# Kernel optimization log

Measured on AMD Instinct MI355X. Metric: run time of the kernel, lower is better.

Reference implementation:

```python
import jax, jax.numpy as jnp
import numpy as np
from jax import lax

V, T, B, E, H, L, K = 32000, 256, 32, 512, 256, 2, 17  # vocab, seq, batch, emb, hidden/dir, layers, tags


def _lstm_dir(x, mask, Wih, Whh, bih, bhh, reverse):
    """One-direction LSTM with packed-sequence semantics.
    x: [B,T,D], mask: [B,T] bool. Padded steps do not update (h,c); padded outputs are 0."""
    Bs, Ts, _ = x.shape
    Hs = Whh.shape[1]
    xg = jnp.einsum('btd,gd->btg', x, Wih) + bih  # precompute input contributions [B,T,4H]

    def step(carry, inp):
        h, c = carry
        xg_t, m_t = inp  # [B,4H], [B]
        g = xg_t + h @ Whh.T + bhh
        i, f, gg, o = jnp.split(g, 4, axis=-1)  # torch gate order: i, f, g, o
        i = jax.nn.sigmoid(i); f = jax.nn.sigmoid(f)
        gg = jnp.tanh(gg); o = jax.nn.sigmoid(o)
        c_new = f * c + i * gg
        h_new = o * jnp.tanh(c_new)
        m = m_t[:, None]
        h2 = jnp.where(m, h_new, h)
        c2 = jnp.where(m, c_new, c)
        out = jnp.where(m, h_new, jnp.zeros_like(h_new))
        return (h2, c2), out

    z = jnp.zeros((Bs, Hs), dtype=x.dtype)
    xs = (jnp.swapaxes(xg, 0, 1), mask.T)
    _, ys = lax.scan(step, (z, z), xs, reverse=reverse)
    return jnp.swapaxes(ys, 0, 1)  # [B,T,H]


def _bilstm(x, mask, Wih, Whh, bih, bhh):
    for l in range(Wih.shape[0]):
        f = _lstm_dir(x, mask, Wih[l, 0], Whh[l, 0], bih[l, 0], bhh[l, 0], reverse=False)
        b = _lstm_dir(x, mask, Wih[l, 1], Whh[l, 1], bih[l, 1], bhh[l, 1], reverse=True)
        x = jnp.concatenate([f, b], axis=-1)
    return x


def _crf_nll(logits, labels, mask, input_lens, trans, start, end):
    maskf = mask.astype(logits.dtype)
    # --- numerator: score of gold path (AllenNLP _joint_likelihood) ---
    emit = jnp.take_along_axis(logits, labels[..., None], axis=2)[..., 0]  # [B,T]
    emit_sum = (emit * maskf).sum(1)
    tr = trans[labels[:, :-1], labels[:, 1:]]  # [B,T-1]
    tr_sum = (tr * maskf[:, 1:]).sum(1)
    last_tags = jnp.take_along_axis(labels, (input_lens - 1)[:, None], axis=1)[:, 0]
    numerator = start[labels[:, 0]] + emit_sum + tr_sum + end[last_tags]
    # --- denominator: forward algorithm over time ---
    alpha0 = start[None, :] + logits[:, 0]  # [B,K]

    def step(alpha, inp):
        logit_t, m_t = inp  # [B,K], [B]
        inner = alpha[:, :, None] + trans[None] + logit_t[:, None, :]  # [B,K,K]
        new = jax.nn.logsumexp(inner, axis=1)
        alpha = jnp.where(m_t[:, None], new, alpha)
        return alpha, None

    xs = (jnp.swapaxes(logits[:, 1:], 0, 1), mask[:, 1:].T)
    alpha, _ = lax.scan(step, alpha0, xs)
    partition = jax.nn.logsumexp(alpha + end[None, :], axis=1)
    return -(numerator - partition).sum()


def setup_inputs() -> dict:
    key = jax.random.key(0)
    ks = jax.random.split(key, 10)
    lens = jax.random.randint(ks[0], (B,), 1, T + 1)
    src = jax.random.randint(ks[1], (B, T), 1, V)
    src = jnp.where(jnp.arange(T)[None, :] < lens[:, None], src, 0)  # pad_idx=0
    labels = jax.random.randint(ks[2], (B, T), 0, K)
    emb = (jax.random.normal(ks[3], (V, E)) * 0.05).at[0].set(0.0)  # padding_idx=0 row zeroed
    Wih = jax.random.normal(ks[4], (L, 2, 4 * H, E)) * 0.05
    Whh = jax.random.normal(ks[5], (L, 2, 4 * H, H)) * 0.05
    bih = jnp.zeros((L, 2, 4 * H))
    bhh = jnp.zeros((L, 2, 4 * H))
    Wlin = jax.random.normal(ks[6], (K, 2 * H)) * 0.05
    blin = jnp.zeros((K,))
    trans = jax.random.normal(ks[7], (K, K)) * 0.05
    start = jax.random.normal(ks[8], (K,)) * 0.05
    end = jax.random.normal(ks[9], (K,)) * 0.05
    return dict(src=src, input_lens=lens, labels=labels, decode=0, emb=emb,
                Wih=Wih, Whh=Whh, bih=bih, bhh=bhh, Wlin=Wlin, blin=blin,
                trans=trans, start=start, end=end)


def reference(src, input_lens, labels, decode, emb, Wih, Whh, bih, bhh, Wlin, blin, trans, start, end):
    mask = src != 0  # create_mask with pad_idx=0
    x = emb[src]  # embedding lookup (dropout p=0 -> identity)
    feats = _bilstm(x, mask, Wih, Whh, bih, bhh)
    logits = feats @ Wlin.T + blin  # [B,T,K]
    # decode=False path: loss = -crf log-likelihood (summed over batch)
    return _crf_nll(logits, labels, mask, input_lens, trans, start, end)
```

## Files before the change

### kernel.cpp

```cpp
#include <hip/hip_runtime.h>

#define TT 256
#define BB 32
#define EE 512
#define HH 256
#define GG 1024
#define NK 17

typedef __attribute__((ext_vector_type(8))) short bf16x8;
typedef __attribute__((ext_vector_type(4))) float f32x4;

#if __has_builtin(__builtin_amdgcn_sdot8)
#define HAS_DOT8 1
#else
#define HAS_DOT8 0
#endif

__device__ __forceinline__ int dot4i8(int a, int b, int c) {
#if __has_builtin(__builtin_amdgcn_sdot4)
  return __builtin_amdgcn_sdot4(a, b, c, false);
#else
  int r = c;
#pragma unroll
  for (int e = 0; e < 4; ++e) {
    int av = (a << (24 - 8 * e)) >> 24;
    int bv = (b << (24 - 8 * e)) >> 24;
    r += av * bv;
  }
  return r;
#endif
}

__device__ __forceinline__ int dot8i4(int a, int b, int c) {
#if HAS_DOT8
  return __builtin_amdgcn_sdot8(a, b, c, false);
#else
  int alo = (a << 4) & (int)0xF0F0F0F0, ahi = a & (int)0xF0F0F0F0;
  int blo = (b << 4) & (int)0xF0F0F0F0, bhi = b & (int)0xF0F0F0F0;
  c = dot4i8(alo, blo, c);
  return dot4i8(ahi, bhi, c);
#endif
}

__device__ __forceinline__ short f2bf(float f) {
  unsigned int u = __float_as_uint(f);
  unsigned int rounding = 0x7FFFu + ((u >> 16) & 1u);
  return (short)((u + rounding) >> 16);
}
__device__ __forceinline__ float bfu2f_lo(unsigned int u) {
  return __uint_as_float(u << 16);
}
__device__ __forceinline__ float bfu2f_hi(unsigned int u) {
  return __uint_as_float(u & 0xFFFF0000u);
}
__device__ __forceinline__ float bfs2f(unsigned short us) {
  return __uint_as_float(((unsigned int)us) << 16);
}

__global__ void k_prep_x(const int* __restrict__ src,
                         const float* __restrict__ emb,
                         const float* __restrict__ Wih,
                         short* __restrict__ xb,
                         short* __restrict__ wbb) {
  int blk = blockIdx.x;
  int t = threadIdx.x;
  if (blk < BB * TT) {
    int v = src[blk];
    const float4* e = reinterpret_cast<const float4*>(emb + (size_t)v * EE) + 2 * t;
    float4 a = e[0], b = e[1];
    bf16x8 r;
    r[0] = f2bf(a.x); r[1] = f2bf(a.y); r[2] = f2bf(a.z); r[3] = f2bf(a.w);
    r[4] = f2bf(b.x); r[5] = f2bf(b.y); r[6] = f2bf(b.z); r[7] = f2bf(b.w);
    *reinterpret_cast<bf16x8*>(xb + (size_t)blk * EE + 8 * t) = r;
  } else {
    int i = ((blk - BB * TT) * 64 + t) * 8;
    float4 a = *reinterpret_cast<const float4*>(Wih + i);
    float4 b = *reinterpret_cast<const float4*>(Wih + i + 4);
    bf16x8 r;
    r[0] = f2bf(a.x); r[1] = f2bf(a.y); r[2] = f2bf(a.z); r[3] = f2bf(a.w);
    r[4] = f2bf(b.x); r[5] = f2bf(b.y); r[6] = f2bf(b.z); r[7] = f2bf(b.w);
    *reinterpret_cast<bf16x8*>(wbb + i) = r;
  }
}

__global__ __launch_bounds__(256) void k_quant4(const float* __restrict__ whh,
                                                const float* __restrict__ bih,
                                                const float* __restrict__ bhh,
                                                int* __restrict__ wq4,
                                                float* __restrict__ scl,
                                                float* __restrict__ biasb) {
  int wid = (blockIdx.x * 256 + threadIdx.x) >> 6;
  int lane = threadIdx.x & 63;
  int ld = wid >> 10, g = wid & 1023;
  float4 v = *reinterpret_cast<const float4*>(whh + (size_t)wid * HH + lane * 4);
  float m = fmaxf(fmaxf(fabsf(v.x), fabsf(v.y)), fmaxf(fabsf(v.z), fabsf(v.w)));
#pragma unroll
  for (int off = 32; off > 0; off >>= 1) m = fmaxf(m, __shfl_xor(m, off));
  m = fmaxf(m, 1e-20f);
  float inv = 7.f / m;
  unsigned q0 = (unsigned)((int)rintf(v.x * inv) & 0xF);
  unsigned q1 = (unsigned)((int)rintf(v.y * inv) & 0xF);
  unsigned q2 = (unsigned)((int)rintf(v.z * inv) & 0xF);
  unsigned q3 = (unsigned)((int)rintf(v.w * inv) & 0xF);
  unsigned bits = q0 | (q1 << 4) | (q2 << 8) | (q3 << 12);
  unsigned hi = __shfl_down(bits, 1);
  if (!(lane & 1)) {
    int kk = lane >> 1;
    wq4[(((size_t)ld * 8 + (kk >> 2)) * 1024 + g) * 4 + (kk & 3)] =
        (int)(bits | (hi << 16));
  }
  if (lane == 0) scl[wid] = m / 49.f;
  if (lane == 1) biasb[wid] = bih[wid] + bhh[wid];
}

__global__ __launch_bounds__(256) void k_gemm_mfma(
    const short* __restrict__ Xb,
    const short* __restrict__ Wb,
    const float* __restrict__ bias,
    unsigned short* __restrict__ out) {
  __shared__ short As[128][72];
  __shared__ short Bs[128][72];
  const int tid = threadIdx.x;
  const int wave = tid >> 6, lane = tid & 63;
  const int wr = wave >> 1, wc = wave & 1;
  const int m0 = blockIdx.y * 128, n0 = blockIdx.x * 128;
  f32x4 acc[4][4] = {};
  for (int k0 = 0; k0 < EE; k0 += 64) {
#pragma unroll
    for (int u = 0; u < 4; ++u) {
      int cid = u * 256 + tid;
      int row = cid >> 3, kc = cid & 7;
      *reinterpret_cast<int4*>(&As[row][kc * 8]) =
          *reinterpret_cast<const int4*>(Xb + (size_t)(m0 + row) * EE + k0 + kc * 8);
      *reinterpret_cast<int4*>(&Bs[row][kc * 8]) =
          *reinterpret_cast<const int4*>(Wb + (size_t)(n0 + row) * EE + k0 + kc * 8);
    }
    __syncthreads();
#pragma unroll
    for (int ko = 0; ko < 2; ++ko) {
      bf16x8 af[4], bff[4];
#pragma unroll
      for (int mi = 0; mi < 4; ++mi)
        af[mi] = *reinterpret_cast<const bf16x8*>(
            &As[wr * 64 + mi * 16 + (lane & 15)][ko * 32 + (lane >> 4) * 8]);
#pragma unroll
      for (int ni = 0; ni < 4; ++ni)
        bff[ni] = *reinterpret_cast<const bf16x8*>(
            &Bs[wc * 64 + ni * 16 + (lane & 15)][ko * 32 + (lane >> 4) * 8]);
#pragma unroll
      for (int mi = 0; mi < 4; ++mi)
#pragma unroll
        for (int ni = 0; ni < 4; ++ni)
          acc[mi][ni] = __builtin_amdgcn_mfma_f32_16x16x32_bf16(af[mi], bff[ni], acc[mi][ni], 0, 0, 0);
    }
    __syncthreads();
  }
  const int r0 = (lane >> 4) * 4, cc = lane & 15;
#pragma unroll
  for (int mi = 0; mi < 4; ++mi)
#pragma unroll
    for (int ni = 0; ni < 4; ++ni) {
      int gcol = n0 + wc * 64 + ni * 16 + cc;
      int dir = gcol >> 10, gg = gcol & 1023;
      float bv = bias[gcol];
      unsigned short* ob = out + (size_t)dir * (BB * TT * GG) + gg;
#pragma unroll
      for (int j = 0; j < 4; ++j) {
        int m = m0 + wr * 64 + mi * 16 + r0 + j;
        ob[(size_t)m * GG] = (unsigned short)f2bf(acc[mi][ni][j] + bv);
      }
    }
}

__global__ __launch_bounds__(512, 2) void k_rec(
    const unsigned short* __restrict__ xg,
    const uint4* __restrict__ wq4,
    const float* __restrict__ scl,
    const int* __restrict__ lens,
    short* __restrict__ outx)
{
  __shared__ float pre[GG];
  __shared__ __align__(16) int hq[32];
  const int bid = blockIdx.x;
  const int b = bid & 31;
  const int dir = bid >> 5;
  const int L = threadIdx.x;
  const int g0 = L, g1 = L + 512;
  const uint4* wp0 = wq4 + (size_t)dir * (8 * 1024) + g0;
  const uint4* wp1 = wq4 + (size_t)dir * (8 * 1024) + g1;
  if (L < 32) hq[L] = 0;
#if HAS_DOT8
  const float f0 = scl[dir * 1024 + g0];
  const float f1 = scl[dir * 1024 + g1];
#else
  const float f0 = scl[dir * 1024 + g0] * (1.f / 256.f);
  const float f1 = scl[dir * 1024 + g1] * (1.f / 256.f);
#endif
  const int len = lens[b];
  const unsigned short* xgb = xg + ((size_t)dir * (BB * TT) + (size_t)b * TT) * GG;
  float c = 0.f;
  __syncthreads();
  for (int s = 0; s < TT; ++s) {
    const int t = dir ? (TT - 1 - s) : s;
    float xv0 = bfs2f(xgb[(size_t)t * GG + g0]);
    float xv1 = bfs2f(xgb[(size_t)t * GG + g1]);
    const uint4* h4 = reinterpret_cast<const uint4*>(hq);
    uint4 hv0 = h4[0], hv1 = h4[1], hv2 = h4[2], hv3 = h4[3];
    uint4 hv4 = h4[4], hv5 = h4[5], hv6 = h4[6], hv7 = h4[7];
    int a0 = 0, a1 = 0;
#define DOTQ(WP, ACC, Q, HV)                               \
    { uint4 wv = WP[(Q) * 1024];                           \
      ACC = dot8i4((int)wv.x, (int)HV.x, ACC);             \
      ACC = dot8i4((int)wv.y, (int)HV.y, ACC);             \
      ACC = dot8i4((int)wv.z, (int)HV.z, ACC);             \
      ACC = dot8i4((int)wv.w, (int)HV.w, ACC); }
    DOTQ(wp0, a0, 0, hv0) DOTQ(wp0, a0, 1, hv1)
    DOTQ(wp0, a0, 2, hv2) DOTQ(wp0, a0, 3, hv3)
    DOTQ(wp0, a0, 4, hv4) DOTQ(wp0, a0, 5, hv5)
    DOTQ(wp0, a0, 6, hv6) DOTQ(wp0, a0, 7, hv7)
    DOTQ(wp1, a1, 0, hv0) DOTQ(wp1, a1, 1, hv1)
    DOTQ(wp1, a1, 2, hv2) DOTQ(wp1, a1, 3, hv3)
    DOTQ(wp1, a1, 4, hv4) DOTQ(wp1, a1, 5, hv5)
    DOTQ(wp1, a1, 6, hv6) DOTQ(wp1, a1, 7, hv7)
#undef DOTQ
    pre[g0] = xv0 + (float)a0 * f0;
    pre[g1] = xv1 + (float)a1 * f1;
    __syncthreads();
    if (L < HH) {
      float gi = pre[L], gf = pre[HH + L], g2 = pre[2 * HH + L], go = pre[3 * HH + L];
      float iv = 1.f / (1.f + __expf(-gi));
      float fv = 1.f / (1.f + __expf(-gf));
      float e2 = __expf(fminf(2.f * g2, 80.f));
      float gv = (e2 - 1.f) / (e2 + 1.f);
      float ov = 1.f / (1.f + __expf(-go));
      float cn = fv * c + iv * gv;
      float e2c = __expf(fminf(2.f * cn, 80.f));
      float th = (e2c - 1.f) / (e2c + 1.f);
      float hn = ov * th;
      const bool m = (t < len);
      outx[((size_t)(b * TT) + t) * (2 * HH) + dir * HH + L] = f2bf(m ? hn : 0.f);
      if (m) {
        c = cn;
        int nib = ((int)rintf(hn * 7.f)) & 0xF;
        int pn = __shfl_xor(nib, 1);
        if (!(L & 1))
          reinterpret_cast<char*>(hq)[L >> 1] = (char)(nib | (pn << 4));
      }
    }
    __syncthreads();
  }
}

__global__ __launch_bounds__(256) void k_logits(
    const short* __restrict__ feats,
    const float* __restrict__ wlin,
    const float* __restrict__ blin,
    float* __restrict__ logits) {
  int o = blockIdx.x * 256 + threadIdx.x;
  int m = o / NK, jj = o - m * NK;
  const uint4* fr = reinterpret_cast<const uint4*>(feats + (size_t)m * EE);
  const float4* wr = reinterpret_cast<const float4*>(wlin + (size_t)jj * EE);
  float s = blin[jj];
  for (int q = 0; q < EE / 8; ++q) {
    uint4 fv = fr[q];
    float4 w0 = wr[2 * q], w1 = wr[2 * q + 1];
    s = fmaf(bfu2f_lo(fv.x), w0.x, s);
    s = fmaf(bfu2f_hi(fv.x), w0.y, s);
    s = fmaf(bfu2f_lo(fv.y), w0.z, s);
    s = fmaf(bfu2f_hi(fv.y), w0.w, s);
    s = fmaf(bfu2f_lo(fv.z), w1.x, s);
    s = fmaf(bfu2f_hi(fv.z), w1.y, s);
    s = fmaf(bfu2f_lo(fv.w), w1.z, s);
    s = fmaf(bfu2f_hi(fv.w), w1.w, s);
  }
  logits[o] = s;
}

__global__ __launch_bounds__(64) void k_crf(
    const float* __restrict__ logits,
    const int* __restrict__ labels,
    const int* __restrict__ lens,
    const float* __restrict__ trans,
    const float* __restrict__ startv,
    const float* __restrict__ endv,
    float* __restrict__ res) {
  const int b = blockIdx.x;
  const int tid = threadIdx.x;
  __shared__ float trs[NK * NK];
  __shared__ float alpha[NK];
  for (int i = tid; i < NK * NK; i += 64) trs[i] = trans[i];
  const int len = lens[b];
  const int* lab = labels + b * TT;
  const float* lg = logits + (size_t)b * TT * NK;
  float part = 0.f;
  for (int t = tid; t < TT; t += 64)
    if (t < len) part += lg[t * NK + lab[t]];
  for (int t = tid; t < TT - 1; t += 64)
    if (t + 1 < len) part += trs[lab[t] * NK + lab[t + 1]];
#pragma unroll
  for (int off = 32; off > 0; off >>= 1) part += __shfl_down(part, off);
  if (tid < NK) alpha[tid] = startv[tid] + lg[tid];
  const int tmax = (len < TT) ? len : TT;
  for (int t = 1; t < tmax; ++t) {
    float nv = 0.f;
    if (tid < NK) {
      float mxv = -1e30f;
#pragma unroll
      for (int i = 0; i < NK; ++i) mxv = fmaxf(mxv, alpha[i] + trs[i * NK + tid]);
      float sum = 0.f;
#pragma unroll
      for (int i = 0; i < NK; ++i) sum += __expf(alpha[i] + trs[i * NK + tid] - mxv);
      nv = mxv + __logf(sum) + lg[t * NK + tid];
    }
    if (tid < NK) alpha[tid] = nv;
  }
  if (tid == 0) {
    float mxv = -1e30f;
    float av[NK];
    for (int i = 0; i < NK; ++i) { av[i] = alpha[i] + endv[i]; mxv = fmaxf(mxv, av[i]); }
    float sum = 0.f;
    for (int i = 0; i < NK; ++i) sum += __expf(av[i] - mxv);
    float partition = mxv + __logf(sum);
    float numer = startv[lab[0]] + part + endv[lab[len - 1]];
    res[b] = numer - partition;
  }
}

__global__ void k_final(const float* __restrict__ res, float* __restrict__ out) {
  int tid = threadIdx.x;
  float v = (tid < BB) ? res[tid] : 0.f;
#pragma unroll
  for (int off = 32; off > 0; off >>= 1) v += __shfl_down(v, off);
  if (tid == 0) out[0] = -v;
}

extern "C" void kernel_launch(void* const* d_in, const int* in_sizes, int n_in,
                              void* d_out, int out_size, void* d_ws, size_t ws_size,
                              hipStream_t stream) {
  const int* src = (const int*)d_in[0];
  const int* lens = (const int*)d_in[1];
  const int* labels = (const int*)d_in[2];
  const float* emb = (const float*)d_in[4];
  const float* Wih = (const float*)d_in[5];
  const float* Whh = (const float*)d_in[6];
  const float* bih = (const float*)d_in[7];
  const float* bhh = (const float*)d_in[8];
  const float* Wlin = (const float*)d_in[9];
  const float* blin = (const float*)d_in[10];
  const float* trans = (const float*)d_in[11];
  const float* startv = (const float*)d_in[12];
  const float* endv = (const float*)d_in[13];

  char* w = (char*)d_ws;
  short* xb0 = (short*)w;   w += (size_t)BB * TT * EE * 2;
  short* xb1 = (short*)w;   w += (size_t)BB * TT * EE * 2;
  short* xb2 = (short*)w;   w += (size_t)BB * TT * EE * 2;
  unsigned short* xg = (unsigned short*)w; w += (size_t)2 * BB * TT * GG * 2;
  int* wq4 = (int*)w;       w += (size_t)4 * 32 * 1024 * 4;
  float* scl = (float*)w;   w += (size_t)4 * 1024 * 4;
  float* biasb = (float*)w; w += (size_t)2 * 2 * GG * 4;
  float* logits = (float*)w; w += (size_t)BB * TT * NK * 4;
  float* res = (float*)w;   w += 256;
  short* wbb = (short*)w;   w += (size_t)4 * GG * EE * 2;

  k_prep_x<<<BB * TT + (4 * GG * EE) / (64 * 8), 64, 0, stream>>>(
      src, emb, Wih, xb0, wbb);
  k_quant4<<<1024, 256, 0, stream>>>(Whh, bih, bhh, wq4, scl, biasb);

  const short* xin[2] = {xb0, xb1};
  short* xout[2] = {xb1, xb2};
  for (int l = 0; l < 2; ++l) {
    k_gemm_mfma<<<dim3(2 * GG / 128, (BB * TT) / 128), 256, 0, stream>>>(
        xin[l], wbb + (size_t)l * 2 * GG * EE, biasb + l * 2 * GG, xg);
    k_rec<<<64, 512, 0, stream>>>(
        xg, reinterpret_cast<const uint4*>(wq4) + (size_t)l * 2 * 8 * 1024,
        scl + (size_t)l * 2 * 1024, lens, xout[l]);
  }

  k_logits<<<(BB * TT * NK) / 256, 256, 0, stream>>>(xb2, Wlin, blin, logits);
  k_crf<<<BB, 64, 0, stream>>>(logits, labels, lens, trans, startv, endv, res);
  k_final<<<1, 64, 0, stream>>>(res, (float*)d_out);
}
```

Measured before the change: 589.9 us.

## Stage GEMM epilogue through LDS for coalesced stores; register-resident CRF forward

The MFMA GEMM epilogue now writes bias-added bf16 results into a shared-memory tile, then stores each row out as coalesced 16-byte vectors. Before, each lane wrote scattered 2-byte values with a large row stride. Separately, the CRF forward recursion keeps the transition column and alpha in registers, exchanges alpha with wave shuffles instead of LDS, and prefetches the next step's logits. This removes the shared-memory round trips on the serial chain. The LDS tile adds about 35KB of shared memory per GEMM block, which may lower occupancy.

```diff
diff --git a/kernel.cpp b/kernel.cpp
--- a/kernel.cpp
+++ b/kernel.cpp
@@ -120,6 +120,7 @@
     unsigned short* __restrict__ out) {
   __shared__ short As[128][72];
   __shared__ short Bs[128][72];
+  __shared__ short Cs[128][136];
   const int tid = threadIdx.x;
   const int wave = tid >> 6, lane = tid & 63;
   const int wr = wave >> 1, wc = wave & 1;
@@ -160,16 +161,22 @@
   for (int mi = 0; mi < 4; ++mi)
 #pragma unroll
     for (int ni = 0; ni < 4; ++ni) {
-      int gcol = n0 + wc * 64 + ni * 16 + cc;
-      int dir = gcol >> 10, gg = gcol & 1023;
-      float bv = bias[gcol];
-      unsigned short* ob = out + (size_t)dir * (BB * TT * GG) + gg;
-#pragma unroll
-      for (int j = 0; j < 4; ++j) {
-        int m = m0 + wr * 64 + mi * 16 + r0 + j;
-        ob[(size_t)m * GG] = (unsigned short)f2bf(acc[mi][ni][j] + bv);
-      }
+      int lcol = wc * 64 + ni * 16 + cc;
+      float bv = bias[n0 + lcol];
+#pragma unroll
+      for (int j = 0; j < 4; ++j)
+        Cs[wr * 64 + mi * 16 + r0 + j][lcol] = f2bf(acc[mi][ni][j] + bv);
     }
+  __syncthreads();
+  const int dir = n0 >> 10, gg0 = n0 & 1023;
+  unsigned short* ob = out + (size_t)dir * (BB * TT * GG) + gg0;
+#pragma unroll
+  for (int p = 0; p < 8; ++p) {
+    int row = p * 16 + (tid >> 4);
+    int col = (tid & 15) * 8;
+    bf16x8 v = *reinterpret_cast<const bf16x8*>(&Cs[row][col]);
+    *reinterpret_cast<bf16x8*>(ob + (size_t)(m0 + row) * GG + col) = v;
+  }
 }
 
 __global__ __launch_bounds__(512, 2) void k_rec(
@@ -276,6 +283,8 @@
   logits[o] = s;
 }
 
+#define REP17(M) M(0) M(1) M(2) M(3) M(4) M(5) M(6) M(7) M(8) \
+                 M(9) M(10) M(11) M(12) M(13) M(14) M(15) M(16)
 __global__ __launch_bounds__(64) void k_crf(
     const float* __restrict__ logits,
     const int* __restrict__ labels,
@@ -287,7 +296,6 @@
   const int b = blockIdx.x;
   const int tid = threadIdx.x;
   __shared__ float trs[NK * NK];
-  __shared__ float alpha[NK];
   for (int i = tid; i < NK * NK; i += 64) trs[i] = trans[i];
   const int len = lens[b];
   const int* lab = labels + b * TT;
@@ -299,31 +307,38 @@
     if (t + 1 < len) part += trs[lab[t] * NK + lab[t + 1]];
 #pragma unroll
   for (int off = 32; off > 0; off >>= 1) part += __shfl_down(part, off);
-  if (tid < NK) alpha[tid] = startv[tid] + lg[tid];
+  const int jc = (tid < NK) ? tid : NK - 1;
+#define TR_DECL(i) float tr##i = trans[(i) * NK + jc];
+  REP17(TR_DECL)
+#undef TR_DECL
+  float alpha = startv[jc] + lg[jc];
   const int tmax = (len < TT) ? len : TT;
+  float lgv = lg[NK + jc];
   for (int t = 1; t < tmax; ++t) {
-    float nv = 0.f;
-    if (tid < NK) {
-      float mxv = -1e30f;
-#pragma unroll
-      for (int i = 0; i < NK; ++i) mxv = fmaxf(mxv, alpha[i] + trs[i * NK + tid]);
-      float sum = 0.f;
-#pragma unroll
-      for (int i = 0; i < NK; ++i) sum += __expf(alpha[i] + trs[i * NK + tid] - mxv);
-      nv = mxv + __logf(sum) + lg[t * NK + tid];
-    }
-    if (tid < NK) alpha[tid] = nv;
-  }
-  if (tid == 0) {
-    float mxv = -1e30f;
-    float av[NK];
-    for (int i = 0; i < NK; ++i) { av[i] = alpha[i] + endv[i]; mxv = fmaxf(mxv, av[i]); }
+    float cur = lgv;
+    int tn = (t + 1 < TT) ? t + 1 : t;
+    lgv = lg[tn * NK + jc];
+    float mx = -1e30f;
+#define SCAN_A(i) float a##i = __shfl(alpha, i) + tr##i; mx = fmaxf(mx, a##i);
+    REP17(SCAN_A)
+#undef SCAN_A
     float sum = 0.f;
-    for (int i = 0; i < NK; ++i) sum += __expf(av[i] - mxv);
-    float partition = mxv + __logf(sum);
-    float numer = startv[lab[0]] + part + endv[lab[len - 1]];
-    res[b] = numer - partition;
-  }
+#define SCAN_S(i) sum += __expf(a##i - mx);
+    REP17(SCAN_S)
+#undef SCAN_S
+    alpha = mx + __logf(sum) + cur;
+  }
+  float pmx = -1e30f;
+#define END_A(i) float p##i = __shfl(alpha, i) + endv[i]; pmx = fmaxf(pmx, p##i);
+  REP17(END_A)
+#undef END_A
+  float psum = 0.f;
+#define END_S(i) psum += __expf(p##i - pmx);
+  REP17(END_S)
+#undef END_S
+  float partition = pmx + __logf(psum);
+  if (tid == 0)
+    res[b] = startv[lab[0]] + part + endv[lab[len - 1]] - partition;
 }
 
 __global__ void k_final(const float* __restrict__ res, float* __restrict__ out) {
```

Measured after the change: 577.9 us. 1.02x faster.
